# Kernel tuning notes

Measured on AMD Instinct MI355X. Metric: run time of the kernel, lower is better.

Reference implementation:

```python
import jax, jax.numpy as jnp
import numpy as np

EPS = 1e-5


def setup_inputs() -> dict:
    key = jax.random.key(0)
    ks = jax.random.split(key, 5)
    N, E, D, L = 10000, 160000, 512, 3
    x = jax.random.normal(ks[0], (N, D), dtype=jnp.float32)
    src = jax.random.randint(ks[1], (E,), 0, N, dtype=jnp.int64)
    dst = jax.random.randint(ks[2], (E,), 0, N, dtype=jnp.int64)
    gamma = jnp.ones((L, D), dtype=jnp.float32)
    beta = jnp.zeros((L, D), dtype=jnp.float32)
    # glorot-ish scale so ReLU stack stays well-conditioned
    W = jax.random.normal(ks[3], (L, D, D), dtype=jnp.float32) * (1.0 / np.sqrt(D))
    b = jnp.zeros((L, D), dtype=jnp.float32)
    return {"x": x, "src": src, "dst": dst, "gamma": gamma, "beta": beta, "W": W, "b": b}


def reference(x, src, dst, gamma, beta, W, b):
    N = x.shape[0]
    ones = jnp.ones(src.shape[0], dtype=x.dtype)
    # DGL GraphConv norm='both': src side uses out-degree, dst side uses in-degree
    out_deg = jnp.clip(jax.ops.segment_sum(ones, src, num_segments=N), 1.0)
    in_deg = jnp.clip(jax.ops.segment_sum(ones, dst, num_segments=N), 1.0)
    src_norm = (out_deg ** -0.5)[:, None]  # [N,1]
    dst_norm = (in_deg ** -0.5)[:, None]   # [N,1]
    n_layers = gamma.shape[0]
    for i in range(n_layers):
        # BatchNorm1d (training mode: batch mean, biased variance)
        mu = jnp.mean(x, axis=0)
        var = jnp.var(x, axis=0)
        x = (x - mu) * jax.lax.rsqrt(var + EPS) * gamma[i] + beta[i]
        h = x * src_norm
        agg = jax.ops.segment_sum(h[src], dst, num_segments=N) * dst_norm
        x = jax.nn.relu(agg @ W[i] + b[i])
    return x
```

## Files before the change

### kernel.cpp

```cpp
#include <hip/hip_runtime.h>
#include <hip/hip_bf16.h>

constexpr int N = 10000;
constexpr int D = 512;
constexpr int E = 160000;
constexpr int L = 3;
constexpr float EPS = 1e-5f;

typedef _Float16 half8 __attribute__((ext_vector_type(8)));
typedef _Float16 half2v __attribute__((ext_vector_type(2)));
typedef float floatx4 __attribute__((ext_vector_type(4)));

__device__ __forceinline__ void glds16(const _Float16* g, _Float16* l) {
    __builtin_amdgcn_global_load_lds(
        (const __attribute__((address_space(1))) uint32_t*)(g),
        (__attribute__((address_space(3))) uint32_t*)(l),
        16, 0, 0);
}

constexpr int DEG_BLOCKS  = (E + 255) / 256;
constexpr int CONV_BLOCKS = 100;
constexpr int TW_BLOCKS   = L * 256;
constexpr int MEGA_BLOCKS = DEG_BLOCKS + CONV_BLOCKS + TW_BLOCKS;

__global__ __launch_bounds__(256) void mega_setup(
    const int* __restrict__ src, const int* __restrict__ dst,
    const float* __restrict__ x, const float* __restrict__ W,
    int* __restrict__ out_deg, int* __restrict__ in_deg,
    _Float16* __restrict__ x16, float* __restrict__ stats0,
    _Float16* __restrict__ Wt) {
    __shared__ float tb[32][33];
    int bid = blockIdx.x;
    int tid = threadIdx.x;
    if (bid < DEG_BLOCKS) {
        int e = bid * 256 + tid;
        if (e < E) {
            atomicAdd(&out_deg[src[e]], 1);
            atomicAdd(&in_deg[dst[e]], 1);
        }
    } else if (bid < DEG_BLOCKS + CONV_BLOCKS) {
        int b = bid - DEG_BLOCKS;
        int r0 = b * 100;
        int r1 = r0 + 100; if (r1 > N) r1 = N;
        int c2 = tid * 2;
        float s0 = 0.f, s1 = 0.f, q0 = 0.f, q1 = 0.f;
        for (int r = r0; r < r1; ++r) {
            float2 v = *(const float2*)(x + (size_t)r * D + c2);
            s0 += v.x; q0 += v.x * v.x;
            s1 += v.y; q1 += v.y * v.y;
            half2v h; h[0] = (_Float16)v.x; h[1] = (_Float16)v.y;
            *(half2v*)(x16 + (size_t)r * D + c2) = h;
        }
        atomicAdd(&stats0[c2], s0);
        atomicAdd(&stats0[c2 + 1], s1);
        atomicAdd(&stats0[D + c2], q0);
        atomicAdd(&stats0[D + c2 + 1], q1);
    } else {
        int b = bid - DEG_BLOCKS - CONV_BLOCKS;
        int l = b >> 8;
        int t = b & 255;
        int k0 = (t >> 4) * 32, n0 = (t & 15) * 32;
        int tx = tid & 31, ty = tid >> 5;
        const float* Wl = W + (size_t)l * D * D;
        _Float16* Wtl = Wt + (size_t)l * D * D;
        for (int i = 0; i < 32; i += 8)
            tb[ty + i][tx] = Wl[(size_t)(k0 + ty + i) * D + n0 + tx];
        __syncthreads();
        for (int i = 0; i < 32; i += 8)
            Wtl[(size_t)(n0 + ty + i) * D + k0 + tx] = (_Float16)tb[tx][ty + i];
    }
}

__global__ void scan_indeg(const int* __restrict__ in_deg,
                           const int* __restrict__ out_deg,
                           int* __restrict__ off, int* __restrict__ cursor,
                           float* __restrict__ src_norm, float* __restrict__ dst_norm) {
    __shared__ int lsum[1024];
    int t = threadIdx.x;
    const int chunk = (N + 1023) / 1024;
    int start = t * chunk;
    int end = start + chunk; if (end > N) end = N;
    int s = 0;
    for (int i = start; i < end; ++i) s += in_deg[i];
    lsum[t] = s;
    __syncthreads();
    for (int d = 1; d < 1024; d <<= 1) {
        int v = (t >= d) ? lsum[t - d] : 0;
        __syncthreads();
        lsum[t] += v;
        __syncthreads();
    }
    int excl = (t == 0) ? 0 : lsum[t - 1];
    for (int i = start; i < end; ++i) {
        off[i] = excl;
        cursor[i] = excl;
        excl += in_deg[i];
        int od = out_deg[i]; if (od < 1) od = 1;
        int id = in_deg[i];  if (id < 1) id = 1;
        src_norm[i] = rsqrtf((float)od);
        dst_norm[i] = rsqrtf((float)id);
    }
    if (t == 1023) off[N] = lsum[1023];
}

__global__ void csr_fill(const int* __restrict__ src, const int* __restrict__ dst,
                         int* __restrict__ cursor, int* __restrict__ csr_src) {
    int e = blockIdx.x * blockDim.x + threadIdx.x;
    if (e >= E) return;
    int d = dst[e];
    int pos = atomicAdd(&cursor[d], 1);
    csr_src[pos] = src[e];
}

__global__ __launch_bounds__(256) void aggregate_bn(
    const _Float16* __restrict__ x, const int* __restrict__ off,
    const int* __restrict__ csr_src, const float* __restrict__ src_norm,
    const float* __restrict__ dst_norm, const float* __restrict__ stats,
    const float* __restrict__ gamma, const float* __restrict__ beta,
    _Float16* __restrict__ agg) {
    int wid = (blockIdx.x * 256 + threadIdx.x) >> 6;
    if (wid >= N) return;
    int lane = threadIdx.x & 63;
    int c0 = lane * 8;

    float scale[8], shift[8];
    const float invN = 1.0f / (float)N;
    for (int i = 0; i < 8; ++i) {
        int c = c0 + i;
        float mu = stats[c] * invN;
        float var = stats[D + c] * invN - mu * mu;
        float sc = gamma[c] * rsqrtf(var + EPS);
        scale[i] = sc;
        shift[i] = beta[c] - mu * sc;
    }

    int e0 = off[wid], e1 = off[wid + 1];
    float a[8] = {}, a2[8] = {};
    float t = 0.f;
    int e = e0;
    for (; e + 4 <= e1; e += 4) {
        int s0 = csr_src[e];
        int s1 = csr_src[e + 1];
        int s2 = csr_src[e + 2];
        int s3 = csr_src[e + 3];
        float n0 = src_norm[s0];
        float n1 = src_norm[s1];
        float n2 = src_norm[s2];
        float n3 = src_norm[s3];
        half8 v0 = *(const half8*)(x + (size_t)s0 * D + c0);
        half8 v1 = *(const half8*)(x + (size_t)s1 * D + c0);
        half8 v2 = *(const half8*)(x + (size_t)s2 * D + c0);
        half8 v3 = *(const half8*)(x + (size_t)s3 * D + c0);
        t += (n0 + n1) + (n2 + n3);
        for (int k = 0; k < 8; ++k) {
            a[k]  += (float)v0[k] * n0;
            a2[k] += (float)v1[k] * n1;
            a[k]  += (float)v2[k] * n2;
            a2[k] += (float)v3[k] * n3;
        }
    }
    for (; e < e1; ++e) {
        int s0 = csr_src[e];
        float n0 = src_norm[s0];
        half8 v0 = *(const half8*)(x + (size_t)s0 * D + c0);
        t += n0;
        for (int k = 0; k < 8; ++k) a[k] += (float)v0[k] * n0;
    }
    float dn = dst_norm[wid];
    half8 o;
    for (int i = 0; i < 8; ++i)
        o[i] = (_Float16)(dn * (scale[i] * (a[i] + a2[i]) + shift[i] * t));
    *(half8*)(agg + (size_t)wid * D + c0) = o;
}

template <typename OutT, bool STATS>
__global__ __launch_bounds__(256) void mm_f16_relu(
    const _Float16* __restrict__ A, const _Float16* __restrict__ Bt,
    const float* __restrict__ bias, OutT* __restrict__ C, int M,
    float* __restrict__ stats) {
    __shared__ __align__(16) _Float16 As[128 * 32];
    __shared__ __align__(16) _Float16 Bs[128 * 32];
    const int tid  = threadIdx.x;
    const int wave = tid >> 6;
    const int lane = tid & 63;
    const int quad = lane >> 4;
    const int l16  = lane & 15;
    const int row0 = blockIdx.x * 128;
    const int col0 = blockIdx.y * 128;
    const int wm = (wave & 1) * 64;
    const int wn = (wave >> 1) * 64;
    const int sr = lane >> 2;
    const int sc = (lane & 3) * 8;

    int ar0 = row0 + wave * 32 + sr;
    int ar1 = ar0 + 16;
    if (ar0 >= M) ar0 = M - 1;
    if (ar1 >= M) ar1 = M - 1;
    const _Float16* gA0 = A + (size_t)ar0 * D + sc;
    const _Float16* gA1 = A + (size_t)ar1 * D + sc;
    const _Float16* gB0 = Bt + (size_t)(col0 + wave * 32 + sr) * D + sc;
    const _Float16* gB1 = Bt + (size_t)(col0 + wave * 32 + 16 + sr) * D + sc;
    _Float16* lA0 = As + (wave * 32) * 32;
    _Float16* lA1 = As + (wave * 32 + 16) * 32;
    _Float16* lB0 = Bs + (wave * 32) * 32;
    _Float16* lB1 = Bs + (wave * 32 + 16) * 32;

    floatx4 acc[4][4] = {};

    for (int k0 = 0; k0 < D; k0 += 32) {
        __syncthreads();
        glds16(gA0 + k0, lA0);
        glds16(gA1 + k0, lA1);
        glds16(gB0 + k0, lB0);
        glds16(gB1 + k0, lB1);
        __syncthreads();
        half8 af[4], bf[4];
        for (int i = 0; i < 4; ++i)
            af[i] = *(const half8*)(As + (wm + i * 16 + l16) * 32 + quad * 8);
        for (int j = 0; j < 4; ++j)
            bf[j] = *(const half8*)(Bs + (wn + j * 16 + l16) * 32 + quad * 8);
        for (int i = 0; i < 4; ++i)
            for (int j = 0; j < 4; ++j)
                acc[i][j] = __builtin_amdgcn_mfma_f32_16x16x32_f16(
                    af[i], bf[j], acc[i][j], 0, 0, 0);
    }

    float s[4] = {}, q[4] = {};
    for (int i = 0; i < 4; ++i) {
        for (int r = 0; r < 4; ++r) {
            int row = row0 + wm + i * 16 + quad * 4 + r;
            bool valid = row < M;
            for (int j = 0; j < 4; ++j) {
                int col = col0 + wn + j * 16 + l16;
                float v = acc[i][j][r] + bias[col];
                v = v > 0.f ? v : 0.f;
                if (valid) {
                    C[(size_t)row * D + col] = (OutT)v;
                    if (STATS) { s[j] += v; q[j] += v * v; }
                }
            }
        }
    }
    if (STATS) {
        for (int j = 0; j < 4; ++j) {
            float sv = s[j], qv = q[j];
            sv += __shfl_xor(sv, 16); sv += __shfl_xor(sv, 32);
            qv += __shfl_xor(qv, 16); qv += __shfl_xor(qv, 32);
            if (quad == 0) {
                int col = col0 + wn + j * 16 + l16;
                atomicAdd(&stats[col], sv);
                atomicAdd(&stats[D + col], qv);
            }
        }
    }
}

extern "C" void kernel_launch(void* const* d_in, const int* in_sizes, int n_in,
                              void* d_out, int out_size, void* d_ws, size_t ws_size,
                              hipStream_t stream) {
    const float* x_in  = (const float*)d_in[0];
    const int*   src   = (const int*)d_in[1];
    const int*   dst   = (const int*)d_in[2];
    const float* gamma = (const float*)d_in[3];
    const float* beta  = (const float*)d_in[4];
    const float* W     = (const float*)d_in[5];
    const float* b     = (const float*)d_in[6];
    float* out = (float*)d_out;

    char* p = (char*)d_ws;
    _Float16* x16 = (_Float16*)p;  p += (size_t)N * D * 2;
    _Float16* agg = (_Float16*)p;  p += (size_t)N * D * 2;
    _Float16* Wt  = (_Float16*)p;  p += (size_t)L * D * D * 2;
    float* src_norm = (float*)p;   p += (size_t)N * 4;
    float* dst_norm = (float*)p;   p += (size_t)N * 4;
    int* out_deg   = (int*)p;      p += (size_t)N * 4;
    int* in_deg    = (int*)p;      p += (size_t)N * 4;
    float* stats0  = (float*)p;    p += 2 * D * 4;
    float* stats1  = (float*)p;    p += 2 * D * 4;
    float* stats2  = (float*)p;    p += 2 * D * 4;
    int* csr_off   = (int*)p;      p += (size_t)(N + 1) * 4;
    int* cursor    = (int*)p;      p += (size_t)N * 4;
    int* csr_src   = (int*)p;      p += (size_t)E * 4;

    float* stats_in[3] = {stats0, stats1, stats2};

    hipMemsetAsync(out_deg, 0, (2 * (size_t)N + 6 * D) * sizeof(int), stream);
    mega_setup<<<MEGA_BLOCKS, 256, 0, stream>>>(src, dst, x_in, W,
                                                out_deg, in_deg, x16, stats0, Wt);
    scan_indeg<<<1, 1024, 0, stream>>>(in_deg, out_deg, csr_off, cursor,
                                       src_norm, dst_norm);
    csr_fill<<<DEG_BLOCKS, 256, 0, stream>>>(src, dst, cursor, csr_src);

    dim3 mm_grid((N + 127) / 128, D / 128);
    const int agg_blocks = (N + 3) / 4;

    for (int l = 0; l < L; ++l) {
        const float* gl  = gamma + (size_t)l * D;
        const float* bl  = beta + (size_t)l * D;
        const _Float16* Wl = Wt + (size_t)l * D * D;
        const float* bil = b + (size_t)l * D;

        aggregate_bn<<<agg_blocks, 256, 0, stream>>>(
            x16, csr_off, csr_src, src_norm, dst_norm, stats_in[l], gl, bl, agg);
        if (l == L - 1) {
            mm_f16_relu<float, false><<<mm_grid, 256, 0, stream>>>(
                agg, Wl, bil, out, N, nullptr);
        } else {
            mm_f16_relu<_Float16, true><<<mm_grid, 256, 0, stream>>>(
                agg, Wl, bil, x16, N, stats_in[l + 1]);
        }
    }
}
```

Before: 282.3 us.

## Shard aggregation by column slices and double-buffer swizzled GEMM tiles

The gather-aggregate kernel is split into 8 column shards of 64 columns each. Each wave handles one node's shard, with its two half-waves taking alternate edges and combining results by shuffle, so each shard's slice of x can stay cache-resident across the gathers. The GEMM moves to 64x128 tiles with 128 threads, a K-step of 64, double-buffered LDS staging with async global-to-LDS loads, and an XOR swizzle to avoid bank conflicts. In exchange, aggregation now re-reads the CSR indices and norms eight times and issues narrow 4-byte loads, and each half-wave only stores on one half.

```diff
diff --git a/kernel.cpp b/kernel.cpp
--- a/kernel.cpp
+++ b/kernel.cpp
@@ -6,6 +6,9 @@
 constexpr int E = 160000;
 constexpr int L = 3;
 constexpr float EPS = 1e-5f;
+
+constexpr int NSHARD = 8;
+constexpr int SHCOL = D / NSHARD;
 
 typedef _Float16 half8 __attribute__((ext_vector_type(8)));
 typedef _Float16 half2v __attribute__((ext_vector_type(2)));
@@ -112,124 +115,164 @@
     csr_src[pos] = src[e];
 }
 
-__global__ __launch_bounds__(256) void aggregate_bn(
+__global__ __launch_bounds__(256) void aggregate_bn_shard(
     const _Float16* __restrict__ x, const int* __restrict__ off,
     const int* __restrict__ csr_src, const float* __restrict__ src_norm,
     const float* __restrict__ dst_norm, const float* __restrict__ stats,
     const float* __restrict__ gamma, const float* __restrict__ beta,
     _Float16* __restrict__ agg) {
-    int wid = (blockIdx.x * 256 + threadIdx.x) >> 6;
-    if (wid >= N) return;
-    int lane = threadIdx.x & 63;
-    int c0 = lane * 8;
-
-    float scale[8], shift[8];
+    int shard = blockIdx.x & 7;
+    int blk   = blockIdx.x >> 3;
+    int wave  = threadIdx.x >> 6;
+    int wid   = blk * 4 + wave;
+    int lane  = threadIdx.x & 63;
+    int half  = lane >> 5;
+    int cl    = lane & 31;
+    int c0    = shard * SHCOL + cl * 2;
+
     const float invN = 1.0f / (float)N;
-    for (int i = 0; i < 8; ++i) {
-        int c = c0 + i;
-        float mu = stats[c] * invN;
-        float var = stats[D + c] * invN - mu * mu;
-        float sc = gamma[c] * rsqrtf(var + EPS);
-        scale[i] = sc;
-        shift[i] = beta[c] - mu * sc;
-    }
+    float2 sv = *(const float2*)(stats + c0);
+    float2 qv = *(const float2*)(stats + D + c0);
+    float2 gm = *(const float2*)(gamma + c0);
+    float2 bt = *(const float2*)(beta + c0);
+    float mu0 = sv.x * invN, mu1 = sv.y * invN;
+    float var0 = qv.x * invN - mu0 * mu0;
+    float var1 = qv.y * invN - mu1 * mu1;
+    float sc0 = gm.x * rsqrtf(var0 + EPS);
+    float sc1 = gm.y * rsqrtf(var1 + EPS);
+    float sh0 = bt.x - mu0 * sc0;
+    float sh1 = bt.y - mu1 * sc1;
 
     int e0 = off[wid], e1 = off[wid + 1];
-    float a[8] = {}, a2[8] = {};
-    float t = 0.f;
-    int e = e0;
-    for (; e + 4 <= e1; e += 4) {
-        int s0 = csr_src[e];
-        int s1 = csr_src[e + 1];
-        int s2 = csr_src[e + 2];
-        int s3 = csr_src[e + 3];
-        float n0 = src_norm[s0];
-        float n1 = src_norm[s1];
-        float n2 = src_norm[s2];
-        float n3 = src_norm[s3];
-        half8 v0 = *(const half8*)(x + (size_t)s0 * D + c0);
-        half8 v1 = *(const half8*)(x + (size_t)s1 * D + c0);
-        half8 v2 = *(const half8*)(x + (size_t)s2 * D + c0);
-        half8 v3 = *(const half8*)(x + (size_t)s3 * D + c0);
-        t += (n0 + n1) + (n2 + n3);
-        for (int k = 0; k < 8; ++k) {
-            a[k]  += (float)v0[k] * n0;
-            a2[k] += (float)v1[k] * n1;
-            a[k]  += (float)v2[k] * n2;
-            a2[k] += (float)v3[k] * n3;
-        }
-    }
-    for (; e < e1; ++e) {
-        int s0 = csr_src[e];
-        float n0 = src_norm[s0];
-        half8 v0 = *(const half8*)(x + (size_t)s0 * D + c0);
-        t += n0;
-        for (int k = 0; k < 8; ++k) a[k] += (float)v0[k] * n0;
-    }
-    float dn = dst_norm[wid];
-    half8 o;
-    for (int i = 0; i < 8; ++i)
-        o[i] = (_Float16)(dn * (scale[i] * (a[i] + a2[i]) + shift[i] * t));
-    *(half8*)(agg + (size_t)wid * D + c0) = o;
+    const _Float16* xs = x + c0;
+    float a0 = 0.f, a1 = 0.f, b0 = 0.f, b1 = 0.f, tA = 0.f, tB = 0.f;
+    int e = e0 + half;
+    for (; e + 2 < e1; e += 4) {
+        int sA = csr_src[e];
+        int sB = csr_src[e + 2];
+        float nA = src_norm[sA];
+        float nB = src_norm[sB];
+        half2v vA = *(const half2v*)(xs + (size_t)sA * D);
+        half2v vB = *(const half2v*)(xs + (size_t)sB * D);
+        a0 += (float)vA[0] * nA; a1 += (float)vA[1] * nA; tA += nA;
+        b0 += (float)vB[0] * nB; b1 += (float)vB[1] * nB; tB += nB;
+    }
+    for (; e < e1; e += 2) {
+        int sA = csr_src[e];
+        float nA = src_norm[sA];
+        half2v vA = *(const half2v*)(xs + (size_t)sA * D);
+        a0 += (float)vA[0] * nA; a1 += (float)vA[1] * nA; tA += nA;
+    }
+    a0 += b0; a1 += b1;
+    float t = tA + tB;
+    a0 += __shfl_xor(a0, 32);
+    a1 += __shfl_xor(a1, 32);
+    t  += __shfl_xor(t, 32);
+    if (half == 0) {
+        float dn = dst_norm[wid];
+        half2v o;
+        o[0] = (_Float16)(dn * (sc0 * a0 + sh0 * t));
+        o[1] = (_Float16)(dn * (sc1 * a1 + sh1 * t));
+        *(half2v*)(agg + (size_t)wid * D + c0) = o;
+    }
 }
 
 template <typename OutT, bool STATS>
-__global__ __launch_bounds__(256) void mm_f16_relu(
+__global__ __launch_bounds__(128) void mm_f16_relu(
     const _Float16* __restrict__ A, const _Float16* __restrict__ Bt,
     const float* __restrict__ bias, OutT* __restrict__ C, int M,
     float* __restrict__ stats) {
-    __shared__ __align__(16) _Float16 As[128 * 32];
-    __shared__ __align__(16) _Float16 Bs[128 * 32];
+    __shared__ __align__(16) _Float16 As[2][64 * 64];
+    __shared__ __align__(16) _Float16 Bs[2][128 * 64];
     const int tid  = threadIdx.x;
     const int wave = tid >> 6;
     const int lane = tid & 63;
     const int quad = lane >> 4;
     const int l16  = lane & 15;
-    const int row0 = blockIdx.x * 128;
+    const int row0 = blockIdx.x * 64;
     const int col0 = blockIdx.y * 128;
-    const int wm = (wave & 1) * 64;
-    const int wn = (wave >> 1) * 64;
-    const int sr = lane >> 2;
-    const int sc = (lane & 3) * 8;
-
-    int ar0 = row0 + wave * 32 + sr;
-    int ar1 = ar0 + 16;
-    if (ar0 >= M) ar0 = M - 1;
-    if (ar1 >= M) ar1 = M - 1;
-    const _Float16* gA0 = A + (size_t)ar0 * D + sc;
-    const _Float16* gA1 = A + (size_t)ar1 * D + sc;
-    const _Float16* gB0 = Bt + (size_t)(col0 + wave * 32 + sr) * D + sc;
-    const _Float16* gB1 = Bt + (size_t)(col0 + wave * 32 + 16 + sr) * D + sc;
-    _Float16* lA0 = As + (wave * 32) * 32;
-    _Float16* lA1 = As + (wave * 32 + 16) * 32;
-    _Float16* lB0 = Bs + (wave * 32) * 32;
-    _Float16* lB1 = Bs + (wave * 32 + 16) * 32;
+    const int wn   = wave * 64;
+
+    const int srl = lane >> 3;
+    const int sq  = lane & 7;
+    const int sqs = (sq ^ srl) * 8;
+
+    const _Float16* gA[4];
+    const _Float16* gB[8];
+#pragma unroll
+    for (int j = 0; j < 4; ++j) {
+        int ar = row0 + wave * 32 + j * 8 + srl;
+        if (ar >= M) ar = M - 1;
+        gA[j] = A + (size_t)ar * D + sqs;
+    }
+#pragma unroll
+    for (int j = 0; j < 8; ++j) {
+        int br = col0 + wave * 64 + j * 8 + srl;
+        gB[j] = Bt + (size_t)br * D + sqs;
+    }
+
+    const int l7 = l16 & 7;
+    const int swz0 = (quad ^ l7) * 8;
+    const int swz1 = ((4 + quad) ^ l7) * 8;
 
     floatx4 acc[4][4] = {};
 
-    for (int k0 = 0; k0 < D; k0 += 32) {
-        __syncthreads();
-        glds16(gA0 + k0, lA0);
-        glds16(gA1 + k0, lA1);
-        glds16(gB0 + k0, lB0);
-        glds16(gB1 + k0, lB1);
-        __syncthreads();
-        half8 af[4], bf[4];
+    auto stage = [&](int buf, int k0) {
+        _Float16* as = As[buf] + (wave * 32) * 64;
+        _Float16* bs = Bs[buf] + (wave * 64) * 64;
+#pragma unroll
+        for (int j = 0; j < 4; ++j)
+            glds16(gA[j] + k0, as + j * 8 * 64);
+#pragma unroll
+        for (int j = 0; j < 8; ++j)
+            glds16(gB[j] + k0, bs + j * 8 * 64);
+    };
+
+    stage(0, 0);
+    __syncthreads();
+
+    int cur = 0;
+    for (int kt = 0; kt < 8; ++kt) {
+        if (kt < 7) stage(cur ^ 1, (kt + 1) * 64);
+        const _Float16* asb = As[cur];
+        const _Float16* bsb = Bs[cur];
+        half8 af0[4], af1[4], bf0[4], bf1[4];
+#pragma unroll
+        for (int i = 0; i < 4; ++i) {
+            int r = i * 16 + l16;
+            af0[i] = *(const half8*)(asb + r * 64 + swz0);
+            af1[i] = *(const half8*)(asb + r * 64 + swz1);
+        }
+#pragma unroll
+        for (int j = 0; j < 4; ++j) {
+            int r = wn + j * 16 + l16;
+            bf0[j] = *(const half8*)(bsb + r * 64 + swz0);
+            bf1[j] = *(const half8*)(bsb + r * 64 + swz1);
+        }
+#pragma unroll
         for (int i = 0; i < 4; ++i)
-            af[i] = *(const half8*)(As + (wm + i * 16 + l16) * 32 + quad * 8);
-        for (int j = 0; j < 4; ++j)
-            bf[j] = *(const half8*)(Bs + (wn + j * 16 + l16) * 32 + quad * 8);
-        for (int i = 0; i < 4; ++i)
+#pragma unroll
             for (int j = 0; j < 4; ++j)
                 acc[i][j] = __builtin_amdgcn_mfma_f32_16x16x32_f16(
-                    af[i], bf[j], acc[i][j], 0, 0, 0);
+                    af0[i], bf0[j], acc[i][j], 0, 0, 0);
+#pragma unroll
+        for (int i = 0; i < 4; ++i)
+#pragma unroll
+            for (int j = 0; j < 4; ++j)
+                acc[i][j] = __builtin_amdgcn_mfma_f32_16x16x32_f16(
+                    af1[i], bf1[j], acc[i][j], 0, 0, 0);
+        __syncthreads();
+        cur ^= 1;
     }
 
     float s[4] = {}, q[4] = {};
+#pragma unroll
     for (int i = 0; i < 4; ++i) {
+#pragma unroll
         for (int r = 0; r < 4; ++r) {
-            int row = row0 + wm + i * 16 + quad * 4 + r;
+            int row = row0 + i * 16 + quad * 4 + r;
             bool valid = row < M;
+#pragma unroll
             for (int j = 0; j < 4; ++j) {
                 int col = col0 + wn + j * 16 + l16;
                 float v = acc[i][j][r] + bias[col];
@@ -242,6 +285,7 @@
         }
     }
     if (STATS) {
+#pragma unroll
         for (int j = 0; j < 4; ++j) {
             float sv = s[j], qv = q[j];
             sv += __shfl_xor(sv, 16); sv += __shfl_xor(sv, 32);
@@ -291,8 +335,8 @@
                                        src_norm, dst_norm);
     csr_fill<<<DEG_BLOCKS, 256, 0, stream>>>(src, dst, cursor, csr_src);
 
-    dim3 mm_grid((N + 127) / 128, D / 128);
-    const int agg_blocks = (N + 3) / 4;
+    dim3 mm_grid((N + 63) / 64, D / 128);
+    const int agg_blocks = NSHARD * ((N + 3) / 4);
 
     for (int l = 0; l < L; ++l) {
         const float* gl  = gamma + (size_t)l * D;
@@ -300,13 +344,13 @@
         const _Float16* Wl = Wt + (size_t)l * D * D;
         const float* bil = b + (size_t)l * D;
 
-        aggregate_bn<<<agg_blocks, 256, 0, stream>>>(
+        aggregate_bn_shard<<<agg_blocks, 256, 0, stream>>>(
             x16, csr_off, csr_src, src_norm, dst_norm, stats_in[l], gl, bl, agg);
         if (l == L - 1) {
-            mm_f16_relu<float, false><<<mm_grid, 256, 0, stream>>>(
+            mm_f16_relu<float, false><<<mm_grid, 128, 0, stream>>>(
                 agg, Wl, bil, out, N, nullptr);
         } else {
-            mm_f16_relu<_Float16, true><<<mm_grid, 256, 0, stream>>>(
+            mm_f16_relu<_Float16, true><<<mm_grid, 128, 0, stream>>>(
                 agg, Wl, bil, x16, N, stats_in[l + 1]);
         }
     }
```

Measured after the change: 346.0 us. 1.23x slower.
